# Optimization experiments

Hardware: AMD Instinct MI355X
Metric: run time of the kernel (lower is better)

Reference implementation:

```python
import jax, jax.numpy as jnp
import numpy as np
from jax.scipy.special import logsumexp

B, N, D, NUM_CLASSES = 8192, 8192, 256, 64
TEMPERATURE = 1.0


def setup_inputs() -> dict:
    key = jax.random.key(0)
    k1, k2, k3, k4 = jax.random.split(key, 4)
    return {
        "text_features": jax.random.normal(k1, (B, D), dtype=jnp.float32),
        "image_features": jax.random.normal(k2, (N, D), dtype=jnp.float32),
        "t_label": jax.random.randint(k3, (B,), 0, NUM_CLASSES),
        "i_targets": jax.random.randint(k4, (N,), 0, NUM_CLASSES),
    }


def reference(text_features, image_features, t_label, i_targets):
    # logits[i,j] = <text_i, image_j> / T   -> [B, N]
    logits = jnp.matmul(text_features, image_features.T) / TEMPERATURE
    mask = t_label[:, None] == i_targets[None, :]  # [B, N] positives
    neg_inf = jnp.array(-jnp.inf, dtype=logits.dtype)
    # per-row logsumexp over positives of -logits, and over negatives of +logits
    lse_p = logsumexp(jnp.where(mask, -logits, neg_inf), axis=1)
    lse_n = logsumexp(jnp.where(mask, neg_inf, logits), axis=1)
    loss = jnp.mean(jax.nn.softplus(lse_n + lse_p))
    return loss
```

## Files before the change

kernel.cpp:

```cpp
#include <hip/hip_runtime.h>
#include <hip/hip_bf16.h>


#define B_ROWS   8192
#define N_COLS   8192
#define DIM      256
#define CSPLIT   32
#define NTILES   ((N_COLS / CSPLIT) / 32)
#define BLK_ROWS 128
#define THREADS  256

typedef __attribute__((ext_vector_type(8))) short bf16x8;
typedef __attribute__((ext_vector_type(4))) float f32x4;

#if __has_builtin(__builtin_amdgcn_exp2f)
#define EXP2F(x) __builtin_amdgcn_exp2f(x)
#else
#define EXP2F(x) exp2f(x)
#endif
#if __has_builtin(__builtin_amdgcn_logf)
#define LOG2F(x) __builtin_amdgcn_logf(x)
#else
#define LOG2F(x) log2f(x)
#endif

__device__ __forceinline__ unsigned short f2bf(float f) {
    union { float f; unsigned u; } c; c.f = f;
    return (unsigned short)((c.u + 0x7FFFu + ((c.u >> 16) & 1u)) >> 16);
}

__device__ __forceinline__ void stage_tile(const char* bsrc, char* ldsd,
                                           int T, int BUF) {
#pragma unroll
    for (int i_ = 0; i_ < 4; ++i_)
        __builtin_amdgcn_global_load_lds(
            (const __attribute__((address_space(1))) unsigned int*)
                (bsrc + (size_t)T * 16384 + i_ * 4096),
            (__attribute__((address_space(3))) unsigned int*)
                (ldsd + (size_t)BUF * 16384 + i_ * 4096),
            16, 0, 0);
}

__device__ __forceinline__ void epi_one(float y, bool p, float& sn, float& sp) {
    const float u = EXP2F(y - 72.0f);
    sn += u;
    if (p) {
        const float v = EXP2F(-y - 72.0f);
        sp += v;
        sn -= u;
    }
}

__global__ void cvt_all_kernel(const float* __restrict__ text,
                               const float* __restrict__ img,
                               unsigned short* __restrict__ Abf,
                               unsigned short* __restrict__ Bt,
                               float* __restrict__ gsum) {
    const float L2E = 1.4426950408889634f;
    const int i = blockIdx.x * blockDim.x + threadIdx.x;
    if (i < 4096) {
        reinterpret_cast<float4*>(gsum)[i] = float4{0.f, 0.f, 0.f, 0.f};
    }
    if (i < 262144) {
        const float4* src = reinterpret_cast<const float4*>(text) + i * 2;
        float4 v0 = src[0], v1 = src[1];
        unsigned short s[8];
        s[0] = f2bf(v0.x * L2E); s[1] = f2bf(v0.y * L2E);
        s[2] = f2bf(v0.z * L2E); s[3] = f2bf(v0.w * L2E);
        s[4] = f2bf(v1.x * L2E); s[5] = f2bf(v1.y * L2E);
        s[6] = f2bf(v1.z * L2E); s[7] = f2bf(v1.w * L2E);
        reinterpret_cast<bf16x8*>(Abf)[i] = *reinterpret_cast<const bf16x8*>(s);
    } else {
        const int C = i - 262144;
        const int g = C >> 10, c = C & 1023;
        const int col = g * 32 + (c & 31);
        const int k8  = c >> 5;
        const float4* src =
            reinterpret_cast<const float4*>(img + (size_t)col * DIM + k8 * 8);
        float4 v0 = src[0], v1 = src[1];
        unsigned short s[8];
        s[0] = f2bf(v0.x); s[1] = f2bf(v0.y); s[2] = f2bf(v0.z); s[3] = f2bf(v0.w);
        s[4] = f2bf(v1.x); s[5] = f2bf(v1.y); s[6] = f2bf(v1.z); s[7] = f2bf(v1.w);
        reinterpret_cast<bf16x8*>(Bt)[C] = *reinterpret_cast<const bf16x8*>(s);
    }
}

__launch_bounds__(THREADS, 3)
__global__ void fused_gemm_lse(const unsigned short* __restrict__ Abf,
                               const unsigned short* __restrict__ Bt,
                               const int* __restrict__ tlab,
                               const int* __restrict__ itgt,
                               float* __restrict__ gsum_p,
                               float* __restrict__ gsum_n) {
    __shared__ char lds[2 * 16384] __attribute__((aligned(128)));

    const int tid  = threadIdx.x;
    const int lane = tid & 63;
    const int wave = tid >> 6;
    const int l15  = lane & 15;
    const int q    = lane >> 4;
    const int rb   = blockIdx.x * BLK_ROWS + wave * 32;
    const int cb0  = blockIdx.y * (N_COLS / CSPLIT);

    bf16x8 afrag0[8], afrag1[8];
    const bf16x8* arow0 =
        reinterpret_cast<const bf16x8*>(Abf + (size_t)(rb + l15) * DIM) + q;
    const bf16x8* arow1 =
        reinterpret_cast<const bf16x8*>(Abf + (size_t)(rb + 16 + l15) * DIM) + q;
#pragma unroll
    for (int ks = 0; ks < 8; ++ks) {
        afrag0[ks] = arow0[ks * 4];
        afrag1[ks] = arow1[ks * 4];
    }

    int rowcls0[4], rowcls1[4];
#pragma unroll
    for (int j = 0; j < 4; ++j) {
        rowcls0[j] = tlab[rb + q * 4 + j];
        rowcls1[j] = tlab[rb + 16 + q * 4 + j];
    }

    float sump0[4] = {0, 0, 0, 0}, sumn0[4] = {0, 0, 0, 0};
    float sump1[4] = {0, 0, 0, 0}, sumn1[4] = {0, 0, 0, 0};

    const char* bsrc = (const char*)Bt
        + ((size_t)blockIdx.y * NTILES) * 16384 + tid * 16;
    char* ldsd = lds + tid * 16;

    stage_tile(bsrc, ldsd, 0, 0);

    for (int t = 0; t < NTILES; ++t) {
        __syncthreads();
        if (t + 1 < NTILES) stage_tile(bsrc, ldsd, t + 1, (t + 1) & 1);

        const int cc0 = itgt[cb0 + t * 32 + l15];
        const int cc1 = itgt[cb0 + t * 32 + 16 + l15];

        f32x4 acc00 = {0, 0, 0, 0}, acc01 = {0, 0, 0, 0};
        f32x4 acc10 = {0, 0, 0, 0}, acc11 = {0, 0, 0, 0};
        const char* bb = lds + (t & 1) * 16384 + q * 512 + l15 * 16;
#pragma unroll
        for (int ks = 0; ks < 8; ++ks) {
            bf16x8 b0 = *reinterpret_cast<const bf16x8*>(bb + ks * 2048);
            bf16x8 b1 = *reinterpret_cast<const bf16x8*>(bb + ks * 2048 + 256);
            acc00 = __builtin_amdgcn_mfma_f32_16x16x32_bf16(afrag0[ks], b0,
                                                            acc00, 0, 0, 0);
            acc01 = __builtin_amdgcn_mfma_f32_16x16x32_bf16(afrag0[ks], b1,
                                                            acc01, 0, 0, 0);
            acc10 = __builtin_amdgcn_mfma_f32_16x16x32_bf16(afrag1[ks], b0,
                                                            acc10, 0, 0, 0);
            acc11 = __builtin_amdgcn_mfma_f32_16x16x32_bf16(afrag1[ks], b1,
                                                            acc11, 0, 0, 0);
        }

#pragma unroll
        for (int j = 0; j < 4; ++j) {
            epi_one(acc00[j], rowcls0[j] == cc0, sumn0[j], sump0[j]);
            epi_one(acc01[j], rowcls0[j] == cc1, sumn0[j], sump0[j]);
            epi_one(acc10[j], rowcls1[j] == cc0, sumn1[j], sump1[j]);
            epi_one(acc11[j], rowcls1[j] == cc1, sumn1[j], sump1[j]);
        }
    }

#pragma unroll
    for (int j = 0; j < 4; ++j) {
        float vp0 = sump0[j], vn0 = sumn0[j];
        float vp1 = sump1[j], vn1 = sumn1[j];
#pragma unroll
        for (int m = 1; m < 16; m <<= 1) {
            vp0 += __shfl_xor(vp0, m, 64);
            vn0 += __shfl_xor(vn0, m, 64);
            vp1 += __shfl_xor(vp1, m, 64);
            vn1 += __shfl_xor(vn1, m, 64);
        }
        if (l15 == 0) {
            const int row0 = rb + q * 4 + j;
            atomicAdd(&gsum_p[row0], vp0);
            atomicAdd(&gsum_n[row0], vn0);
            const int row1 = rb + 16 + q * 4 + j;
            atomicAdd(&gsum_p[row1], vp1);
            atomicAdd(&gsum_n[row1], vn1);
        }
    }
}

__global__ void finalize_kernel(const float* __restrict__ gsum_p,
                                const float* __restrict__ gsum_n,
                                float* __restrict__ out) {
    __shared__ float red[1024];
    const float LN2 = 0.6931471805599453f;
    const float C2  = 72.0f;
    float acc = 0.f;
    for (int i = threadIdx.x; i < B_ROWS; i += 1024) {
        float zp = (LOG2F(gsum_p[i]) + C2) * LN2;
        float zn = (LOG2F(gsum_n[i]) + C2) * LN2;
        float z  = zp + zn;
        float sp = fmaxf(z, 0.f) + log1pf(expf(-fabsf(z)));
        acc += sp;
    }
    red[threadIdx.x] = acc;
    __syncthreads();
    for (int s = 512; s > 0; s >>= 1) {
        if ((int)threadIdx.x < s) red[threadIdx.x] += red[threadIdx.x + s];
        __syncthreads();
    }
    if (threadIdx.x == 0) out[0] = red[0] / (float)B_ROWS;
}

extern "C" void kernel_launch(void* const* d_in, const int* in_sizes, int n_in,
                              void* d_out, int out_size, void* d_ws, size_t ws_size,
                              hipStream_t stream) {
    const float* text = (const float*)d_in[0];
    const float* img  = (const float*)d_in[1];
    const int* tlab   = (const int*)d_in[2];
    const int* itgt   = (const int*)d_in[3];
    float* out        = (float*)d_out;

    char* ws = (char*)d_ws;
    unsigned short* Abf = (unsigned short*)(ws);
    unsigned short* Bt  = (unsigned short*)(ws + (size_t)B_ROWS * DIM * 2);
    float* gsum_p = (float*)(ws + (size_t)(B_ROWS + N_COLS) * DIM * 2);
    float* gsum_n = gsum_p + B_ROWS;

    cvt_all_kernel<<<(2 * 262144) / 256, 256, 0, stream>>>(text, img, Abf, Bt,
                                                           gsum_p);

    dim3 grid(B_ROWS / BLK_ROWS, CSPLIT);
    fused_gemm_lse<<<grid, THREADS, 0, stream>>>(Abf, Bt, tlab, itgt,
                                                 gsum_p, gsum_n);

    finalize_kernel<<<1, 1024, 0, stream>>>(gsum_p, gsum_n, out);
}
```

Measured before the change: 70.88 us.

## Drop mask from main GEMM epilogue; compute positive pairs in class-bucketed side kernel

The main fused GEMM epilogue no longer loads labels or branches on the class match. It sums exp2 over every column, and a new per-class kernel handles the positive pairs. That kernel buckets rows and columns by label and recomputes only the same-class dot products. From these it accumulates both the positive logsumexp term and the exp sum to subtract from the negatives in the finalize step. This removes per-element compares and the divergent second exponential from the hot loop. The cost is two extra launches, atomic-counter contention when building the lists, gathered loads, and fp32 cancellation in the subtraction. Buckets are capped at 256 entries per class and labels are masked to 64 classes, so skewed label distributions would silently drop pairs.

Result: slower. 155.1 us (+118.8%).

```diff
diff --git a/kernel.cpp b/kernel.cpp
--- a/kernel.cpp
+++ b/kernel.cpp
@@ -9,6 +9,8 @@
 #define NTILES   ((N_COLS / CSPLIT) / 32)
 #define BLK_ROWS 128
 #define THREADS  256
+#define NCLS     64
+#define CLS_CAP  256
 
 typedef __attribute__((ext_vector_type(8))) short bf16x8;
 typedef __attribute__((ext_vector_type(4))) float f32x4;
@@ -41,25 +43,15 @@
             16, 0, 0);
 }
 
-__device__ __forceinline__ void epi_one(float y, bool p, float& sn, float& sp) {
-    const float u = EXP2F(y - 72.0f);
-    sn += u;
-    if (p) {
-        const float v = EXP2F(-y - 72.0f);
-        sp += v;
-        sn -= u;
-    }
-}
-
 __global__ void cvt_all_kernel(const float* __restrict__ text,
                                const float* __restrict__ img,
                                unsigned short* __restrict__ Abf,
                                unsigned short* __restrict__ Bt,
-                               float* __restrict__ gsum) {
+                               float* __restrict__ zero_base) {
     const float L2E = 1.4426950408889634f;
     const int i = blockIdx.x * blockDim.x + threadIdx.x;
-    if (i < 4096) {
-        reinterpret_cast<float4*>(gsum)[i] = float4{0.f, 0.f, 0.f, 0.f};
+    if (i < 6176) {
+        reinterpret_cast<float4*>(zero_base)[i] = float4{0.f, 0.f, 0.f, 0.f};
     }
     if (i < 262144) {
         const float4* src = reinterpret_cast<const float4*>(text) + i * 2;
@@ -85,12 +77,28 @@
     }
 }
 
+__global__ void build_lists_kernel(const int* __restrict__ tlab,
+                                   const int* __restrict__ itgt,
+                                   int* __restrict__ rcnt,
+                                   int* __restrict__ ccnt,
+                                   int* __restrict__ cls_rows,
+                                   int* __restrict__ cls_cols) {
+    const int i = blockIdx.x * blockDim.x + threadIdx.x;
+    if (i < B_ROWS) {
+        const int c = tlab[i] & (NCLS - 1);
+        const int s = atomicAdd(&rcnt[c], 1);
+        if (s < CLS_CAP) cls_rows[c * CLS_CAP + s] = i;
+    } else {
+        const int j = i - B_ROWS;
+        const int c = itgt[j] & (NCLS - 1);
+        const int s = atomicAdd(&ccnt[c], 1);
+        if (s < CLS_CAP) cls_cols[c * CLS_CAP + s] = j;
+    }
+}
+
 __launch_bounds__(THREADS, 3)
 __global__ void fused_gemm_lse(const unsigned short* __restrict__ Abf,
                                const unsigned short* __restrict__ Bt,
-                               const int* __restrict__ tlab,
-                               const int* __restrict__ itgt,
-                               float* __restrict__ gsum_p,
                                float* __restrict__ gsum_n) {
     __shared__ char lds[2 * 16384] __attribute__((aligned(128)));
 
@@ -100,7 +108,6 @@
     const int l15  = lane & 15;
     const int q    = lane >> 4;
     const int rb   = blockIdx.x * BLK_ROWS + wave * 32;
-    const int cb0  = blockIdx.y * (N_COLS / CSPLIT);
 
     bf16x8 afrag0[8], afrag1[8];
     const bf16x8* arow0 =
@@ -113,15 +120,8 @@
         afrag1[ks] = arow1[ks * 4];
     }
 
-    int rowcls0[4], rowcls1[4];
-#pragma unroll
-    for (int j = 0; j < 4; ++j) {
-        rowcls0[j] = tlab[rb + q * 4 + j];
-        rowcls1[j] = tlab[rb + 16 + q * 4 + j];
-    }
-
-    float sump0[4] = {0, 0, 0, 0}, sumn0[4] = {0, 0, 0, 0};
-    float sump1[4] = {0, 0, 0, 0}, sumn1[4] = {0, 0, 0, 0};
+    float sumn0[4] = {0, 0, 0, 0};
+    float sumn1[4] = {0, 0, 0, 0};
 
     const char* bsrc = (const char*)Bt
         + ((size_t)blockIdx.y * NTILES) * 16384 + tid * 16;
@@ -132,9 +132,6 @@
     for (int t = 0; t < NTILES; ++t) {
         __syncthreads();
         if (t + 1 < NTILES) stage_tile(bsrc, ldsd, t + 1, (t + 1) & 1);
-
-        const int cc0 = itgt[cb0 + t * 32 + l15];
-        const int cc1 = itgt[cb0 + t * 32 + 16 + l15];
 
         f32x4 acc00 = {0, 0, 0, 0}, acc01 = {0, 0, 0, 0};
         f32x4 acc10 = {0, 0, 0, 0}, acc11 = {0, 0, 0, 0};
@@ -155,45 +152,144 @@
 
 #pragma unroll
         for (int j = 0; j < 4; ++j) {
-            epi_one(acc00[j], rowcls0[j] == cc0, sumn0[j], sump0[j]);
-            epi_one(acc01[j], rowcls0[j] == cc1, sumn0[j], sump0[j]);
-            epi_one(acc10[j], rowcls1[j] == cc0, sumn1[j], sump1[j]);
-            epi_one(acc11[j], rowcls1[j] == cc1, sumn1[j], sump1[j]);
+            sumn0[j] += EXP2F(acc00[j] - 72.0f) + EXP2F(acc01[j] - 72.0f);
+            sumn1[j] += EXP2F(acc10[j] - 72.0f) + EXP2F(acc11[j] - 72.0f);
         }
     }
 
 #pragma unroll
     for (int j = 0; j < 4; ++j) {
-        float vp0 = sump0[j], vn0 = sumn0[j];
-        float vp1 = sump1[j], vn1 = sumn1[j];
+        float vn0 = sumn0[j], vn1 = sumn1[j];
 #pragma unroll
         for (int m = 1; m < 16; m <<= 1) {
-            vp0 += __shfl_xor(vp0, m, 64);
             vn0 += __shfl_xor(vn0, m, 64);
-            vp1 += __shfl_xor(vp1, m, 64);
             vn1 += __shfl_xor(vn1, m, 64);
         }
         if (l15 == 0) {
-            const int row0 = rb + q * 4 + j;
-            atomicAdd(&gsum_p[row0], vp0);
-            atomicAdd(&gsum_n[row0], vn0);
-            const int row1 = rb + 16 + q * 4 + j;
-            atomicAdd(&gsum_p[row1], vp1);
-            atomicAdd(&gsum_n[row1], vn1);
+            atomicAdd(&gsum_n[rb + q * 4 + j], vn0);
+            atomicAdd(&gsum_n[rb + 16 + q * 4 + j], vn1);
+        }
+    }
+}
+
+__launch_bounds__(THREADS, 2)
+__global__ void mini_pos_kernel(const unsigned short* __restrict__ Abf,
+                                const unsigned short* __restrict__ Bt,
+                                const int* __restrict__ rcnt,
+                                const int* __restrict__ ccnt,
+                                const int* __restrict__ cls_rows,
+                                const int* __restrict__ cls_cols,
+                                float* __restrict__ gsum_p,
+                                float* __restrict__ gsum_pc) {
+    const int c  = blockIdx.x;
+    const int rc = min(rcnt[c], CLS_CAP);
+    const int cn = min(ccnt[c], CLS_CAP);
+    if (rc == 0 || cn == 0) return;
+    const int rt = (rc + 31) >> 5, ct = (cn + 31) >> 5;
+
+    const int tid  = threadIdx.x;
+    const int lane = tid & 63;
+    const int wave = tid >> 6;
+    const int l15  = lane & 15;
+    const int q    = lane >> 4;
+    const int* rl = cls_rows + c * CLS_CAP;
+    const int* cl = cls_cols + c * CLS_CAP;
+
+    int task = 0;
+    for (int a = 0; a < rt; ++a) {
+        for (int b = 0; b < ct; ++b, ++task) {
+            if ((task & 3) != wave) continue;
+
+            const int r0 = rl[min(a * 32 + l15, rc - 1)];
+            const int r1 = rl[min(a * 32 + 16 + l15, rc - 1)];
+            const int c0 = cl[min(b * 32 + l15, cn - 1)];
+            const int c1 = cl[min(b * 32 + 16 + l15, cn - 1)];
+            const bool cv0 = (b * 32 + l15) < cn;
+            const bool cv1 = (b * 32 + 16 + l15) < cn;
+
+            const bf16x8* a0p =
+                reinterpret_cast<const bf16x8*>(Abf + (size_t)r0 * DIM) + q;
+            const bf16x8* a1p =
+                reinterpret_cast<const bf16x8*>(Abf + (size_t)r1 * DIM) + q;
+            const char* b0p = (const char*)Bt + (size_t)(c0 >> 5) * 16384
+                              + (c0 & 31) * 16 + q * 512;
+            const char* b1p = (const char*)Bt + (size_t)(c1 >> 5) * 16384
+                              + (c1 & 31) * 16 + q * 512;
+
+            f32x4 acc00 = {0, 0, 0, 0}, acc01 = {0, 0, 0, 0};
+            f32x4 acc10 = {0, 0, 0, 0}, acc11 = {0, 0, 0, 0};
+#pragma unroll
+            for (int ks = 0; ks < 8; ++ks) {
+                bf16x8 a0 = a0p[ks * 4], a1 = a1p[ks * 4];
+                bf16x8 b0 = *reinterpret_cast<const bf16x8*>(b0p + ks * 2048);
+                bf16x8 b1 = *reinterpret_cast<const bf16x8*>(b1p + ks * 2048);
+                acc00 = __builtin_amdgcn_mfma_f32_16x16x32_bf16(a0, b0, acc00,
+                                                                0, 0, 0);
+                acc01 = __builtin_amdgcn_mfma_f32_16x16x32_bf16(a0, b1, acc01,
+                                                                0, 0, 0);
+                acc10 = __builtin_amdgcn_mfma_f32_16x16x32_bf16(a1, b0, acc10,
+                                                                0, 0, 0);
+                acc11 = __builtin_amdgcn_mfma_f32_16x16x32_bf16(a1, b1, acc11,
+                                                                0, 0, 0);
+            }
+
+#pragma unroll
+            for (int j = 0; j < 4; ++j) {
+                {
+                    const int rp = a * 32 + q * 4 + j;
+                    const bool rv = rp < rc;
+                    const float y0 = acc00[j], y1 = acc01[j];
+                    float uu = ((rv && cv0) ? EXP2F(y0 - 72.0f) : 0.f)
+                             + ((rv && cv1) ? EXP2F(y1 - 72.0f) : 0.f);
+                    float vv = ((rv && cv0) ? EXP2F(-y0 - 72.0f) : 0.f)
+                             + ((rv && cv1) ? EXP2F(-y1 - 72.0f) : 0.f);
+#pragma unroll
+                    for (int m = 1; m < 16; m <<= 1) {
+                        uu += __shfl_xor(uu, m, 64);
+                        vv += __shfl_xor(vv, m, 64);
+                    }
+                    if (l15 == 0 && rv) {
+                        const int rg = rl[rp];
+                        atomicAdd(&gsum_p[rg], vv);
+                        atomicAdd(&gsum_pc[rg], uu);
+                    }
+                }
+                {
+                    const int rp = a * 32 + 16 + q * 4 + j;
+                    const bool rv = rp < rc;
+                    const float y0 = acc10[j], y1 = acc11[j];
+                    float uu = ((rv && cv0) ? EXP2F(y0 - 72.0f) : 0.f)
+                             + ((rv && cv1) ? EXP2F(y1 - 72.0f) : 0.f);
+                    float vv = ((rv && cv0) ? EXP2F(-y0 - 72.0f) : 0.f)
+                             + ((rv && cv1) ? EXP2F(-y1 - 72.0f) : 0.f);
+#pragma unroll
+                    for (int m = 1; m < 16; m <<= 1) {
+                        uu += __shfl_xor(uu, m, 64);
+                        vv += __shfl_xor(vv, m, 64);
+                    }
+                    if (l15 == 0 && rv) {
+                        const int rg = rl[rp];
+                        atomicAdd(&gsum_p[rg], vv);
+                        atomicAdd(&gsum_pc[rg], uu);
+                    }
+                }
+            }
         }
     }
 }
 
 __global__ void finalize_kernel(const float* __restrict__ gsum_p,
                                 const float* __restrict__ gsum_n,
+                                const float* __restrict__ gsum_pc,
                                 float* __restrict__ out) {
     __shared__ float red[1024];
     const float LN2 = 0.6931471805599453f;
     const float C2  = 72.0f;
     float acc = 0.f;
     for (int i = threadIdx.x; i < B_ROWS; i += 1024) {
+        const float sn = fmaxf(gsum_n[i] - gsum_pc[i], 1e-38f);
         float zp = (LOG2F(gsum_p[i]) + C2) * LN2;
-        float zn = (LOG2F(gsum_n[i]) + C2) * LN2;
+        float zn = (LOG2F(sn) + C2) * LN2;
         float z  = zp + zn;
         float sp = fmaxf(z, 0.f) + log1pf(expf(-fabsf(z)));
         acc += sp;
@@ -219,15 +315,27 @@
     char* ws = (char*)d_ws;
     unsigned short* Abf = (unsigned short*)(ws);
     unsigned short* Bt  = (unsigned short*)(ws + (size_t)B_ROWS * DIM * 2);
-    float* gsum_p = (float*)(ws + (size_t)(B_ROWS + N_COLS) * DIM * 2);
-    float* gsum_n = gsum_p + B_ROWS;
+    char* base2 = ws + (size_t)(B_ROWS + N_COLS) * DIM * 2;
+    float* gsum_p  = (float*)(base2);
+    float* gsum_n  = gsum_p + B_ROWS;
+    float* gsum_pc = gsum_n + B_ROWS;
+    int*   rcnt    = (int*)(gsum_pc + B_ROWS);
+    int*   ccnt    = rcnt + NCLS;
+    int*   cls_rows = ccnt + NCLS;
+    int*   cls_cols = cls_rows + NCLS * CLS_CAP;
 
     cvt_all_kernel<<<(2 * 262144) / 256, 256, 0, stream>>>(text, img, Abf, Bt,
                                                            gsum_p);
 
+    build_lists_kernel<<<(2 * B_ROWS) / 256, 256, 0, stream>>>(
+        tlab, itgt, rcnt, ccnt, cls_rows, cls_cols);
+
+    mini_pos_kernel<<<NCLS, THREADS, 0, stream>>>(Abf, Bt, rcnt, ccnt,
+                                                  cls_rows, cls_cols,
+                                                  gsum_p, gsum_pc);
+
     dim3 grid(B_ROWS / BLK_ROWS, CSPLIT);
-    fused_gemm_lse<<<grid, THREADS, 0, stream>>>(Abf, Bt, tlab, itgt,
-                                                 gsum_p, gsum_n);
-
-    finalize_kernel<<<1, 1024, 0, stream>>>(gsum_p, gsum_n, out);
-}
+    fused_gemm_lse<<<grid, THREADS, 0, stream>>>(Abf, Bt, gsum_n);
+
+    finalize_kernel<<<1, 1024, 0, stream>>>(gsum_p, gsum_n, gsum_pc, out);
+}
```
